# Optimization experiments

Hardware: AMD Instinct MI355X
Metric: run time of the kernel (lower is better)

Reference implementation:

```python
import jax, jax.numpy as jnp
import numpy as np

D = 64
H = 4
HD = D // H
N_MOL, E_MOL = 2048, 32768
N_PROT, E_PROT = 8192, 262144
LN_EPS = 1e-5


def _lin_params(key, d_in, d_out):
    k1, k2 = jax.random.split(key)
    lim = 1.0 / np.sqrt(d_in)
    w = jax.random.uniform(k1, (d_in, d_out), minval=-lim, maxval=lim, dtype=jnp.float32)
    b = jax.random.uniform(k2, (d_out,), minval=-lim, maxval=lim, dtype=jnp.float32)
    return w, b


def setup_inputs() -> dict:
    key = jax.random.key(0)
    ks = jax.random.split(key, 20)
    inp = {
        'x_mol': jax.random.normal(ks[0], (N_MOL, D), dtype=jnp.float32),
        'edge_index_mol': jax.random.randint(ks[1], (2, E_MOL), 0, N_MOL),
        'edge_attr_mol': jax.random.normal(ks[2], (E_MOL, D), dtype=jnp.float32),
        'x_prot': jax.random.normal(ks[3], (N_PROT, D), dtype=jnp.float32),
        'edge_index_prot': jax.random.randint(ks[4], (2, E_PROT), 0, N_PROT),
        'edge_attr_prot': jax.random.normal(ks[5], (E_PROT, D), dtype=jnp.float32),
    }
    # GINE MLPs: Linear -> ReLU -> Linear
    inp['mol_w1'], inp['mol_b1'] = _lin_params(ks[6], D, D)
    inp['mol_w2'], inp['mol_b2'] = _lin_params(ks[7], D, D)
    inp['prot_w1'], inp['prot_b1'] = _lin_params(ks[8], D, D)
    inp['prot_w2'], inp['prot_b2'] = _lin_params(ks[9], D, D)
    # cross-attn mol->prot (query=mol, key/value=prot)
    inp['mp_wq'], inp['mp_bq'] = _lin_params(ks[10], D, D)
    inp['mp_wk'], inp['mp_bk'] = _lin_params(ks[11], D, D)
    inp['mp_wv'], inp['mp_bv'] = _lin_params(ks[12], D, D)
    # cross-attn prot->mol (query=prot, key/value=mol)
    inp['pm_wq'], inp['pm_bq'] = _lin_params(ks[13], D, D)
    inp['pm_wk'], inp['pm_bk'] = _lin_params(ks[14], D, D)
    inp['pm_wv'], inp['pm_bv'] = _lin_params(ks[15], D, D)
    # layer norms
    inp['ln_mol_g'] = jnp.ones((D,), jnp.float32)
    inp['ln_mol_b'] = jnp.zeros((D,), jnp.float32)
    inp['ln_prot_g'] = jnp.ones((D,), jnp.float32)
    inp['ln_prot_b'] = jnp.zeros((D,), jnp.float32)
    return inp


def _gine_conv(x, edge_index, edge_attr, w1, b1, w2, b2, n_nodes):
    # message: relu(x_j + edge_attr); aggregate: mean at target; update: MLP((1+eps)*x + aggr), eps=0
    src, dst = edge_index[0], edge_index[1]
    msg = jax.nn.relu(x[src] + edge_attr)                       # [E, D]
    ssum = jax.ops.segment_sum(msg, dst, num_segments=n_nodes)  # [N, D]
    cnt = jax.ops.segment_sum(jnp.ones((msg.shape[0],), msg.dtype), dst, num_segments=n_nodes)
    aggr = ssum / jnp.maximum(cnt, 1.0)[:, None]
    h = x + aggr
    h = jax.nn.relu(h @ w1 + b1) @ w2 + b2
    return h


def _cross_attn(q_nodes, k_nodes, wq, bq, wk, bk, wv, bv):
    Nq, Nk = q_nodes.shape[0], k_nodes.shape[0]
    Q = (q_nodes @ wq + bq).reshape(Nq, H, HD)
    K = (k_nodes @ wk + bk).reshape(Nk, H, HD)
    V = (k_nodes @ wv + bv).reshape(Nk, H, HD)
    scores = jnp.einsum('qhd,khd->hqk', Q, K) / np.sqrt(HD).astype(np.float32)
    attn = jax.nn.softmax(scores, axis=-1)                      # [H, Nq, Nk]
    out = jnp.einsum('hqk,khd->qhd', attn, V).reshape(Nq, D)
    return out


def _layer_norm(x, g, b):
    mu = jnp.mean(x, axis=-1, keepdims=True)
    var = jnp.mean(jnp.square(x - mu), axis=-1, keepdims=True)
    return (x - mu) * jax.lax.rsqrt(var + LN_EPS) * g + b


def reference(x_mol, edge_index_mol, edge_attr_mol, x_prot, edge_index_prot, edge_attr_prot,
              mol_w1, mol_b1, mol_w2, mol_b2, prot_w1, prot_b1, prot_w2, prot_b2,
              mp_wq, mp_bq, mp_wk, mp_bk, mp_wv, mp_bv,
              pm_wq, pm_bq, pm_wk, pm_bk, pm_wv, pm_bv,
              ln_mol_g, ln_mol_b, ln_prot_g, ln_prot_b):
    h_mol = jax.nn.relu(_gine_conv(x_mol, edge_index_mol, edge_attr_mol,
                                   mol_w1, mol_b1, mol_w2, mol_b2, x_mol.shape[0]))
    h_prot = jax.nn.relu(_gine_conv(x_prot, edge_index_prot, edge_attr_prot,
                                    prot_w1, prot_b1, prot_w2, prot_b2, x_prot.shape[0]))
    h_mol_attn = _cross_attn(h_mol, h_prot, mp_wq, mp_bq, mp_wk, mp_bk, mp_wv, mp_bv)
    h_prot_attn = _cross_attn(h_prot, h_mol, pm_wq, pm_bq, pm_wk, pm_bk, pm_wv, pm_bv)
    out_mol = _layer_norm(h_mol + h_mol_attn, ln_mol_g, ln_mol_b)
    out_prot = _layer_norm(h_prot + h_prot_attn, ln_prot_g, ln_prot_b)
    return out_mol, out_prot
```

## Files before the change

kernel.cpp:

```cpp
#include <hip/hip_runtime.h>
#include <hip/hip_bf16.h>

#define NM 2048
#define EM 32768
#define NP 8192
#define EP 262144

typedef __attribute__((ext_vector_type(8))) short short8;
typedef __attribute__((ext_vector_type(4))) float f32x4;

#define LOG2E 1.44269504088896340736f

__device__ __forceinline__ unsigned short cvt_bf16(float f) {
    __hip_bfloat16 h = __float2bfloat16(f);
    return *(unsigned short*)&h;
}
__device__ __forceinline__ unsigned int pk_bf16(float a, float b) {
    unsigned int lo = cvt_bf16(a), hi = cvt_bf16(b);
    return lo | (hi << 16);
}

__global__ __launch_bounds__(256) void hist_kernel(
    const int* __restrict__ ei_m, const int* __restrict__ ei_p,
    int* __restrict__ cnt_m, int* __restrict__ cnt_p)
{
    int idx = blockIdx.x * 256 + threadIdx.x;
    if (idx < EM) atomicAdd(&cnt_m[ei_m[EM + idx]], 1);
    int j = idx - EM;
    if (j >= 0 && j < EP) atomicAdd(&cnt_p[ei_p[EP + j]], 1);
}

__global__ __launch_bounds__(256) void scan_kernel(
    const int* __restrict__ cnt_m, const int* __restrict__ cnt_p,
    int* __restrict__ start_m, int* __restrict__ start_p,
    int* __restrict__ cur_m, int* __restrict__ cur_p)
{
    const int* cnt; int* start; int* cur; int n;
    if (blockIdx.x == 0) { cnt = cnt_m; start = start_m; cur = cur_m; n = NM; }
    else                 { cnt = cnt_p; start = start_p; cur = cur_p; n = NP; }
    int per = n >> 8;
    int tid = threadIdx.x;
    int base = tid * per;
    int s = 0;
    for (int i = 0; i < per; i++) s += cnt[base + i];
    __shared__ int wsum[4];
    int lane = tid & 63, w = tid >> 6;
    int v = s;
    #pragma unroll
    for (int off = 1; off < 64; off <<= 1) {
        int u = __shfl_up(v, off, 64);
        if (lane >= off) v += u;
    }
    if (lane == 63) wsum[w] = v;
    __syncthreads();
    int wo = 0;
    for (int i = 0; i < w; i++) wo += wsum[i];
    int run = wo + v - s;
    for (int i = 0; i < per; i++) {
        start[base + i] = run; cur[base + i] = run;
        run += cnt[base + i];
    }
    if (tid == 255) start[n] = run;
}

__global__ __launch_bounds__(256) void scatter_kernel(
    const int* __restrict__ ei_m, const int* __restrict__ ei_p,
    int* __restrict__ cur_m, int* __restrict__ cur_p,
    int* __restrict__ perm_m, int* __restrict__ perm_p,
    int* __restrict__ srcs_m, int* __restrict__ srcs_p)
{
    int idx = blockIdx.x * 256 + threadIdx.x;
    if (idx < EM) {
        int d = ei_m[EM + idx];
        int pos = atomicAdd(&cur_m[d], 1);
        perm_m[pos] = idx; srcs_m[pos] = ei_m[idx];
    }
    int j = idx - EM;
    if (j >= 0 && j < EP) {
        int d = ei_p[EP + j];
        int pos = atomicAdd(&cur_p[d], 1);
        perm_p[pos] = j; srcs_p[pos] = ei_p[j];
    }
}

__global__ __launch_bounds__(256) void node_aggr_kernel(
    const float* __restrict__ x_m, const float* __restrict__ ea_m,
    const int* __restrict__ start_m, const int* __restrict__ perm_m, const int* __restrict__ srcs_m,
    const float* __restrict__ x_p, const float* __restrict__ ea_p,
    const int* __restrict__ start_p, const int* __restrict__ perm_p, const int* __restrict__ srcs_p,
    float* __restrict__ h0_m, float* __restrict__ h0_p)
{
    int wave = threadIdx.x >> 6, lane = threadIdx.x & 63;
    int nid = blockIdx.x * 4 + wave;
    const float *x, *ea; const int *start, *perm, *srcs; float* h0; int n;
    if (nid < NM) { x = x_m; ea = ea_m; start = start_m; perm = perm_m; srcs = srcs_m; h0 = h0_m; n = nid; }
    else          { x = x_p; ea = ea_p; start = start_p; perm = perm_p; srcs = srcs_p; h0 = h0_p; n = nid - NM; }
    int b = start[n], e = start[n + 1];
    int deg = e - b;
    float acc = 0.f;
    for (int c0 = 0; c0 < deg; c0 += 64) {
        int rem = deg - c0;
        int mcount = rem < 64 ? rem : 64;
        int eL = 0, sL = 0;
        if (lane < mcount) { eL = perm[b + c0 + lane]; sL = srcs[b + c0 + lane]; }
        int j = 0;
        for (; j + 3 < mcount; j += 4) {
            int e0 = __shfl(eL, j, 64),   e1 = __shfl(eL, j + 1, 64);
            int e2 = __shfl(eL, j + 2, 64), e3 = __shfl(eL, j + 3, 64);
            int s0 = __shfl(sL, j, 64),   s1 = __shfl(sL, j + 1, 64);
            int s2 = __shfl(sL, j + 2, 64), s3 = __shfl(sL, j + 3, 64);
            float a0 = ea[(size_t)e0 * 64 + lane], a1 = ea[(size_t)e1 * 64 + lane];
            float a2 = ea[(size_t)e2 * 64 + lane], a3 = ea[(size_t)e3 * 64 + lane];
            float y0 = x[(size_t)s0 * 64 + lane], y1 = x[(size_t)s1 * 64 + lane];
            float y2 = x[(size_t)s2 * 64 + lane], y3 = x[(size_t)s3 * 64 + lane];
            acc += fmaxf(y0 + a0, 0.f);
            acc += fmaxf(y1 + a1, 0.f);
            acc += fmaxf(y2 + a2, 0.f);
            acc += fmaxf(y3 + a3, 0.f);
        }
        for (; j < mcount; ++j) {
            int e0 = __shfl(eL, j, 64);
            int s0 = __shfl(sL, j, 64);
            acc += fmaxf(x[(size_t)s0 * 64 + lane] + ea[(size_t)e0 * 64 + lane], 0.f);
        }
    }
    float aggr = acc / fmaxf((float)deg, 1.f);
    h0[(size_t)n * 64 + lane] = x[(size_t)n * 64 + lane] + aggr;
}

__global__ __launch_bounds__(256) void gine_mlp_kernel(
    const float* __restrict__ h0_m, const float* __restrict__ h0_p,
    const float* __restrict__ w1m, const float* __restrict__ b1m,
    const float* __restrict__ w2m, const float* __restrict__ b2m,
    const float* __restrict__ w1p, const float* __restrict__ b1p,
    const float* __restrict__ w2p, const float* __restrict__ b2p,
    float* __restrict__ hm, float* __restrict__ hp)
{
    const float *h0, *w1, *b1, *w2, *b2; float* out; int row0;
    if (blockIdx.x < NM / 16) {
        h0 = h0_m; w1 = w1m; b1 = b1m; w2 = w2m; b2 = b2m; out = hm;
        row0 = blockIdx.x * 16;
    } else {
        h0 = h0_p; w1 = w1p; b1 = b1p; w2 = w2p; b2 = b2p; out = hp;
        row0 = (blockIdx.x - NM / 16) * 16;
    }
    __shared__ float sW1[4096], sW2[4096], sb1[64], sb2[64];
    __shared__ float sh0[16][64], sh1[16][64];
    int t = threadIdx.x;
    for (int i = t; i < 4096; i += 256) { sW1[i] = w1[i]; sW2[i] = w2[i]; }
    if (t < 64) { sb1[t] = b1[t]; sb2[t] = b2[t]; }
    for (int i = t; i < 16 * 64; i += 256) {
        int r = i >> 6, c = i & 63;
        sh0[r][c] = h0[(size_t)(row0 + r) * 64 + c];
    }
    __syncthreads();
    int j = t & 63, rs = t >> 6;
    for (int r = rs; r < 16; r += 4) {
        float a = sb1[j];
        #pragma unroll
        for (int c = 0; c < 64; c++) a += sh0[r][c] * sW1[c * 64 + j];
        sh1[r][j] = fmaxf(a, 0.0f);
    }
    __syncthreads();
    for (int r = rs; r < 16; r += 4) {
        float a = sb2[j];
        #pragma unroll
        for (int c = 0; c < 64; c++) a += sh1[r][c] * sW2[c * 64 + j];
        out[(size_t)(row0 + r) * 64 + j] = fmaxf(a, 0.0f);
    }
}

__global__ __launch_bounds__(256) void qkv_bf16_kernel(
    const float* __restrict__ hm, const float* __restrict__ hp,
    const float* __restrict__ wq_m, const float* __restrict__ bq_m,
    const float* __restrict__ wk_m, const float* __restrict__ bk_m,
    const float* __restrict__ wv_m, const float* __restrict__ bv_m,
    const float* __restrict__ wq_p, const float* __restrict__ bq_p,
    const float* __restrict__ wk_p, const float* __restrict__ bk_p,
    const float* __restrict__ wv_p, const float* __restrict__ bv_p,
    unsigned short* __restrict__ Qm, unsigned short* __restrict__ Km, unsigned short* __restrict__ Vtm,
    unsigned short* __restrict__ Qp, unsigned short* __restrict__ Kp, unsigned short* __restrict__ Vtp)
{
    const float *x, *wq, *bq, *wk, *bk, *wv, *bv;
    unsigned short *Q, *K, *Vt; int row0, N;
    if (blockIdx.x < NM / 16) {
        x = hm; wq = wq_m; bq = bq_m; wk = wk_m; bk = bk_m; wv = wv_m; bv = bv_m;
        Q = Qm; K = Km; Vt = Vtm; N = NM; row0 = blockIdx.x * 16;
    } else {
        x = hp; wq = wq_p; bq = bq_p; wk = wk_p; bk = bk_p; wv = wv_p; bv = bv_p;
        Q = Qp; K = Kp; Vt = Vtp; N = NP; row0 = (blockIdx.x - NM / 16) * 16;
    }
    __shared__ float sWq[4096], sWk[4096], sWv[4096];
    __shared__ float sbq[64], sbk[64], sbv[64];
    __shared__ float sh0[16][64];
    int t = threadIdx.x;
    for (int i = t; i < 4096; i += 256) { sWq[i] = wq[i]; sWk[i] = wk[i]; sWv[i] = wv[i]; }
    if (t < 64) { sbq[t] = bq[t]; sbk[t] = bk[t]; sbv[t] = bv[t]; }
    for (int i = t; i < 16 * 64; i += 256) {
        int r = i >> 6, c = i & 63;
        sh0[r][c] = x[(size_t)(row0 + r) * 64 + c];
    }
    __syncthreads();
    int j = t & 63, rs = t >> 6;
    for (int r = rs; r < 16; r += 4) {
        float aq = sbq[j], ak = sbk[j], av = sbv[j];
        #pragma unroll
        for (int c = 0; c < 64; c++) {
            float h = sh0[r][c];
            aq += h * sWq[c * 64 + j];
            ak += h * sWk[c * 64 + j];
            av += h * sWv[c * 64 + j];
        }
        size_t o = (size_t)(row0 + r) * 64 + j;
        Q[o] = cvt_bf16(aq * (0.25f * LOG2E));
        K[o] = cvt_bf16(ak);
        Vt[(size_t)j * N + row0 + r] = cvt_bf16(av);
    }
}

__global__ __launch_bounds__(256) void attn_partial_kernel(
    const unsigned short* __restrict__ Q, const unsigned short* __restrict__ K,
    const unsigned short* __restrict__ Vt, float* __restrict__ partial,
    int Nk, int ncbits)
{
    __shared__ unsigned int plds[4][16][20];
    int t = threadIdx.x;
    int wave = t >> 6;
    int lane = t & 63;
    int qrow = lane & 15;
    int quad = lane >> 4;
    int NC = 1 << ncbits;
    int task = blockIdx.x * 4 + wave;
    int chunk = task & (NC - 1);
    int tmp = task >> ncbits;
    int h = tmp & 3;
    int qt = tmp >> 2;

    short8 qf = {};
    if (quad < 2)
        qf = *(const short8*)(Q + ((size_t)(qt * 16 + qrow)) * 64 + h * 16 + quad * 8);

    float m = -3.0e38f, l = 0.0f;
    f32x4 acc = {0.f, 0.f, 0.f, 0.f};
    const f32x4 zero4 = {0.f, 0.f, 0.f, 0.f};
    int kbase = chunk * 1024;
    const unsigned short* vrow = Vt + ((size_t)(h * 16 + qrow)) * Nk;

    short8 kf0n = {}, kf1n = {}, vfn;
    {
        int key0 = kbase;
        if (quad < 2) {
            kf0n = *(const short8*)(K + ((size_t)(key0 + qrow)) * 64 + h * 16 + quad * 8);
            kf1n = *(const short8*)(K + ((size_t)(key0 + 16 + qrow)) * 64 + h * 16 + quad * 8);
        }
        vfn = *(const short8*)(vrow + key0 + quad * 8);
    }

    for (int it = 0; it < 32; ++it) {
        short8 kf0 = kf0n, kf1 = kf1n, vf = vfn;
        if (it < 31) {
            int key0 = kbase + (it + 1) * 32;
            if (quad < 2) {
                kf0n = *(const short8*)(K + ((size_t)(key0 + qrow)) * 64 + h * 16 + quad * 8);
                kf1n = *(const short8*)(K + ((size_t)(key0 + 16 + qrow)) * 64 + h * 16 + quad * 8);
            }
            vfn = *(const short8*)(vrow + key0 + quad * 8);
        }

        f32x4 s0 = __builtin_amdgcn_mfma_f32_16x16x32_bf16(kf0, qf, zero4, 0, 0, 0);
        f32x4 s1 = __builtin_amdgcn_mfma_f32_16x16x32_bf16(kf1, qf, zero4, 0, 0, 0);

        float tmax = fmaxf(fmaxf(fmaxf(s0.x, s0.y), fmaxf(s0.z, s0.w)),
                           fmaxf(fmaxf(s1.x, s1.y), fmaxf(s1.z, s1.w)));
        tmax = fmaxf(tmax, __shfl_xor(tmax, 16, 64));
        tmax = fmaxf(tmax, __shfl_xor(tmax, 32, 64));
        float mnew = fmaxf(m, tmax);
        float alpha = exp2f(m - mnew);
        float p00 = exp2f(s0.x - mnew), p01 = exp2f(s0.y - mnew);
        float p02 = exp2f(s0.z - mnew), p03 = exp2f(s0.w - mnew);
        float p10 = exp2f(s1.x - mnew), p11 = exp2f(s1.y - mnew);
        float p12 = exp2f(s1.z - mnew), p13 = exp2f(s1.w - mnew);
        l = l * alpha + (((p00 + p01) + (p02 + p03)) + ((p10 + p11) + (p12 + p13)));
        acc.x *= alpha; acc.y *= alpha; acc.z *= alpha; acc.w *= alpha;

        plds[wave][qrow][quad * 2]     = pk_bf16(p00, p01);
        plds[wave][qrow][quad * 2 + 1] = pk_bf16(p02, p03);
        plds[wave][qrow][8 + quad * 2]     = pk_bf16(p10, p11);
        plds[wave][qrow][8 + quad * 2 + 1] = pk_bf16(p12, p13);
        short8 pf = *(short8*)&plds[wave][qrow][quad * 4];

        acc = __builtin_amdgcn_mfma_f32_16x16x32_bf16(vf, pf, acc, 0, 0, 0);
        m = mnew;
    }

    float ltot = l + __shfl_xor(l, 16, 64);
    ltot += __shfl_xor(ltot, 32, 64);

    float* pb = partial + (size_t)task * 288;
    *(f32x4*)&pb[qrow * 16 + quad * 4] = acc;
    if (quad == 0) { pb[256 + qrow] = m; pb[272 + qrow] = ltot; }
}

__global__ __launch_bounds__(256) void merge_ln_kernel(
    const float* __restrict__ partial, const float* __restrict__ hbuf,
    const float* __restrict__ g, const float* __restrict__ bia,
    float* __restrict__ out, int NC)
{
    int row = blockIdx.x * 4 + (threadIdx.x >> 6);
    int c = threadIdx.x & 63;
    int hi = c >> 4, d = c & 15;
    int qt = row >> 4, ql = row & 15;
    const float* base = partial + (size_t)(qt * 4 + hi) * NC * 288;
    float M = -3.0e38f;
    for (int cc = 0; cc < NC; ++cc) M = fmaxf(M, base[cc * 288 + 256 + ql]);
    float L = 0.0f, A = 0.0f;
    for (int cc = 0; cc < NC; ++cc) {
        float w = exp2f(base[cc * 288 + 256 + ql] - M);
        L += base[cc * 288 + 272 + ql] * w;
        A += base[cc * 288 + ql * 16 + d] * w;
    }
    float v = hbuf[(size_t)row * 64 + c] + A / L;
    float s = v;
    #pragma unroll
    for (int o = 32; o >= 1; o >>= 1) s += __shfl_xor(s, o, 64);
    float mu = s * (1.0f / 64.0f);
    float dv = v - mu;
    float sq = dv * dv;
    #pragma unroll
    for (int o = 32; o >= 1; o >>= 1) sq += __shfl_xor(sq, o, 64);
    float var = sq * (1.0f / 64.0f);
    out[(size_t)row * 64 + c] = dv * rsqrtf(var + 1e-5f) * g[c] + bia[c];
}

extern "C" void kernel_launch(void* const* d_in, const int* in_sizes, int n_in,
                              void* d_out, int out_size, void* d_ws, size_t ws_size,
                              hipStream_t stream)
{
    const float* x_mol   = (const float*)d_in[0];
    const int*   ei_mol  = (const int*)  d_in[1];
    const float* ea_mol  = (const float*)d_in[2];
    const float* x_prot  = (const float*)d_in[3];
    const int*   ei_prot = (const int*)  d_in[4];
    const float* ea_prot = (const float*)d_in[5];
    const float* mol_w1  = (const float*)d_in[6];
    const float* mol_b1  = (const float*)d_in[7];
    const float* mol_w2  = (const float*)d_in[8];
    const float* mol_b2  = (const float*)d_in[9];
    const float* prot_w1 = (const float*)d_in[10];
    const float* prot_b1 = (const float*)d_in[11];
    const float* prot_w2 = (const float*)d_in[12];
    const float* prot_b2 = (const float*)d_in[13];
    const float* mp_wq = (const float*)d_in[14]; const float* mp_bq = (const float*)d_in[15];
    const float* mp_wk = (const float*)d_in[16]; const float* mp_bk = (const float*)d_in[17];
    const float* mp_wv = (const float*)d_in[18]; const float* mp_bv = (const float*)d_in[19];
    const float* pm_wq = (const float*)d_in[20]; const float* pm_bq = (const float*)d_in[21];
    const float* pm_wk = (const float*)d_in[22]; const float* pm_bk = (const float*)d_in[23];
    const float* pm_wv = (const float*)d_in[24]; const float* pm_bv = (const float*)d_in[25];
    const float* ln_mol_g  = (const float*)d_in[26];
    const float* ln_mol_b  = (const float*)d_in[27];
    const float* ln_prot_g = (const float*)d_in[28];
    const float* ln_prot_b = (const float*)d_in[29];

    float* ws = (float*)d_ws;
    float* h_mol   = ws;
    float* h_prot  = h_mol + 131072;
    float* partial = h_prot + 524288;
    float* h0_mol  = partial;
    float* h0_prot = h0_mol + 131072;
    int* ip      = (int*)(partial + 1179648);
    int* cnt_m   = ip;
    int* cnt_p   = cnt_m + 2048;
    int* start_m = cnt_p + 8192;
    int* start_p = start_m + 2052;
    int* cur_m   = start_p + 8196;
    int* cur_p   = cur_m + 2048;
    int* perm_m  = cur_p + 8192;
    int* perm_p  = perm_m + 32768;
    int* srcs_m  = perm_p + 262144;
    int* srcs_p  = srcs_m + 32768;
    unsigned short* bf = (unsigned short*)(srcs_p + 262144);
    unsigned short* Qm  = bf;
    unsigned short* Km  = Qm + 131072;
    unsigned short* Vtm = Km + 131072;
    unsigned short* Qp  = Vtm + 131072;
    unsigned short* Kp  = Qp + 524288;
    unsigned short* Vtp = Kp + 524288;

    hipMemsetAsync(cnt_m, 0, (size_t)(2048 + 8192) * sizeof(int), stream);

    const int EB = (EM + EP) / 256;
    hist_kernel<<<EB, 256, 0, stream>>>(ei_mol, ei_prot, cnt_m, cnt_p);
    scan_kernel<<<2, 256, 0, stream>>>(cnt_m, cnt_p, start_m, start_p, cur_m, cur_p);
    scatter_kernel<<<EB, 256, 0, stream>>>(ei_mol, ei_prot, cur_m, cur_p, perm_m, perm_p, srcs_m, srcs_p);
    node_aggr_kernel<<<(NM + NP) / 4, 256, 0, stream>>>(
        x_mol, ea_mol, start_m, perm_m, srcs_m,
        x_prot, ea_prot, start_p, perm_p, srcs_p, h0_mol, h0_prot);

    gine_mlp_kernel<<<(NM + NP) / 16, 256, 0, stream>>>(
        h0_mol, h0_prot, mol_w1, mol_b1, mol_w2, mol_b2,
        prot_w1, prot_b1, prot_w2, prot_b2, h_mol, h_prot);

    qkv_bf16_kernel<<<(NM + NP) / 16, 256, 0, stream>>>(
        h_mol, h_prot,
        mp_wq, mp_bq, pm_wk, pm_bk, pm_wv, pm_bv,
        pm_wq, pm_bq, mp_wk, mp_bk, mp_wv, mp_bv,
        Qm, Km, Vtm, Qp, Kp, Vtp);

    float* out = (float*)d_out;

    attn_partial_kernel<<<1024, 256, 0, stream>>>(Qm, Kp, Vtp, partial, NP, 3);
    merge_ln_kernel<<<NM / 4, 256, 0, stream>>>(partial, h_mol, ln_mol_g, ln_mol_b, out, 8);

    attn_partial_kernel<<<1024, 256, 0, stream>>>(Qp, Km, Vtm, partial, NM, 1);
    merge_ln_kernel<<<NP / 4, 256, 0, stream>>>(partial, h_prot, ln_prot_g, ln_prot_b, out + 131072, 2);
}
```

Before: 333.2 us.

## Fuse both attention directions and merges into single launches; pack edge indices

```diff
diff --git a/kernel.cpp b/kernel.cpp
--- a/kernel.cpp
+++ b/kernel.cpp
@@ -1,5 +1,4 @@
 #include <hip/hip_runtime.h>
-#include <hip/hip_bf16.h>
 
 #define NM 2048
 #define EM 32768
@@ -11,13 +10,16 @@
 
 #define LOG2E 1.44269504088896340736f
 
+__device__ __forceinline__ float e2(float x) { return __builtin_amdgcn_exp2f(x); }
+__device__ __forceinline__ unsigned int pk_bf16(float a, float b) {
+    unsigned int ua = __float_as_uint(a) + 0x8000u;
+    unsigned int ub = __float_as_uint(b) + 0x8000u;
+    return __builtin_amdgcn_perm(ua, ub, 0x03020706u);
+}
 __device__ __forceinline__ unsigned short cvt_bf16(float f) {
-    __hip_bfloat16 h = __float2bfloat16(f);
-    return *(unsigned short*)&h;
-}
-__device__ __forceinline__ unsigned int pk_bf16(float a, float b) {
-    unsigned int lo = cvt_bf16(a), hi = cvt_bf16(b);
-    return lo | (hi << 16);
+    unsigned int u = __float_as_uint(f);
+    u = (u + 0x7fff + ((u >> 16) & 1)) >> 16;
+    return (unsigned short)u;
 }
 
 __global__ __launch_bounds__(256) void hist_kernel(
@@ -66,62 +68,62 @@
 __global__ __launch_bounds__(256) void scatter_kernel(
     const int* __restrict__ ei_m, const int* __restrict__ ei_p,
     int* __restrict__ cur_m, int* __restrict__ cur_p,
-    int* __restrict__ perm_m, int* __restrict__ perm_p,
-    int* __restrict__ srcs_m, int* __restrict__ srcs_p)
+    int* __restrict__ pidx_m, int* __restrict__ pidx_p)
 {
     int idx = blockIdx.x * 256 + threadIdx.x;
     if (idx < EM) {
         int d = ei_m[EM + idx];
         int pos = atomicAdd(&cur_m[d], 1);
-        perm_m[pos] = idx; srcs_m[pos] = ei_m[idx];
+        pidx_m[pos] = (idx << 11) | ei_m[idx];
     }
     int j = idx - EM;
     if (j >= 0 && j < EP) {
         int d = ei_p[EP + j];
         int pos = atomicAdd(&cur_p[d], 1);
-        perm_p[pos] = j; srcs_p[pos] = ei_p[j];
+        pidx_p[pos] = (j << 13) | ei_p[j];
     }
 }
 
 __global__ __launch_bounds__(256) void node_aggr_kernel(
     const float* __restrict__ x_m, const float* __restrict__ ea_m,
-    const int* __restrict__ start_m, const int* __restrict__ perm_m, const int* __restrict__ srcs_m,
+    const int* __restrict__ start_m, const int* __restrict__ pidx_m,
     const float* __restrict__ x_p, const float* __restrict__ ea_p,
-    const int* __restrict__ start_p, const int* __restrict__ perm_p, const int* __restrict__ srcs_p,
+    const int* __restrict__ start_p, const int* __restrict__ pidx_p,
     float* __restrict__ h0_m, float* __restrict__ h0_p)
 {
     int wave = threadIdx.x >> 6, lane = threadIdx.x & 63;
     int nid = blockIdx.x * 4 + wave;
-    const float *x, *ea; const int *start, *perm, *srcs; float* h0; int n;
-    if (nid < NM) { x = x_m; ea = ea_m; start = start_m; perm = perm_m; srcs = srcs_m; h0 = h0_m; n = nid; }
-    else          { x = x_p; ea = ea_p; start = start_p; perm = perm_p; srcs = srcs_p; h0 = h0_p; n = nid - NM; }
+    const float *x, *ea; const int *start, *pidx; float* h0; int n, sh, msk;
+    if (nid < NM) { x = x_m; ea = ea_m; start = start_m; pidx = pidx_m; h0 = h0_m; n = nid; sh = 11; msk = 2047; }
+    else          { x = x_p; ea = ea_p; start = start_p; pidx = pidx_p; h0 = h0_p; n = nid - NM; sh = 13; msk = 8191; }
     int b = start[n], e = start[n + 1];
     int deg = e - b;
     float acc = 0.f;
     for (int c0 = 0; c0 < deg; c0 += 64) {
         int rem = deg - c0;
         int mcount = rem < 64 ? rem : 64;
-        int eL = 0, sL = 0;
-        if (lane < mcount) { eL = perm[b + c0 + lane]; sL = srcs[b + c0 + lane]; }
+        int pk = 0;
+        if (lane < mcount) pk = pidx[b + c0 + lane];
         int j = 0;
         for (; j + 3 < mcount; j += 4) {
-            int e0 = __shfl(eL, j, 64),   e1 = __shfl(eL, j + 1, 64);
-            int e2 = __shfl(eL, j + 2, 64), e3 = __shfl(eL, j + 3, 64);
-            int s0 = __shfl(sL, j, 64),   s1 = __shfl(sL, j + 1, 64);
-            int s2 = __shfl(sL, j + 2, 64), s3 = __shfl(sL, j + 3, 64);
-            float a0 = ea[(size_t)e0 * 64 + lane], a1 = ea[(size_t)e1 * 64 + lane];
-            float a2 = ea[(size_t)e2 * 64 + lane], a3 = ea[(size_t)e3 * 64 + lane];
-            float y0 = x[(size_t)s0 * 64 + lane], y1 = x[(size_t)s1 * 64 + lane];
-            float y2 = x[(size_t)s2 * 64 + lane], y3 = x[(size_t)s3 * 64 + lane];
+            int v0 = __shfl(pk, j, 64),     v1 = __shfl(pk, j + 1, 64);
+            int v2 = __shfl(pk, j + 2, 64), v3 = __shfl(pk, j + 3, 64);
+            float a0 = ea[(size_t)(((unsigned)v0) >> sh) * 64 + lane];
+            float a1 = ea[(size_t)(((unsigned)v1) >> sh) * 64 + lane];
+            float a2 = ea[(size_t)(((unsigned)v2) >> sh) * 64 + lane];
+            float a3 = ea[(size_t)(((unsigned)v3) >> sh) * 64 + lane];
+            float y0 = x[(size_t)(v0 & msk) * 64 + lane];
+            float y1 = x[(size_t)(v1 & msk) * 64 + lane];
+            float y2 = x[(size_t)(v2 & msk) * 64 + lane];
+            float y3 = x[(size_t)(v3 & msk) * 64 + lane];
             acc += fmaxf(y0 + a0, 0.f);
             acc += fmaxf(y1 + a1, 0.f);
             acc += fmaxf(y2 + a2, 0.f);
             acc += fmaxf(y3 + a3, 0.f);
         }
         for (; j < mcount; ++j) {
-            int e0 = __shfl(eL, j, 64);
-            int s0 = __shfl(sL, j, 64);
-            acc += fmaxf(x[(size_t)s0 * 64 + lane] + ea[(size_t)e0 * 64 + lane], 0.f);
+            int v0 = __shfl(pk, j, 64);
+            acc += fmaxf(x[(size_t)(v0 & msk) * 64 + lane] + ea[(size_t)(((unsigned)v0) >> sh) * 64 + lane], 0.f);
         }
     }
     float aggr = acc / fmaxf((float)deg, 1.f);
@@ -218,10 +220,12 @@
     }
 }
 
-__global__ __launch_bounds__(256) void attn_partial_kernel(
-    const unsigned short* __restrict__ Q, const unsigned short* __restrict__ K,
-    const unsigned short* __restrict__ Vt, float* __restrict__ partial,
-    int Nk, int ncbits)
+__global__ __launch_bounds__(256) void attn_kernel(
+    const unsigned short* __restrict__ Qm, const unsigned short* __restrict__ Km,
+    const unsigned short* __restrict__ Vtm,
+    const unsigned short* __restrict__ Qp, const unsigned short* __restrict__ Kp,
+    const unsigned short* __restrict__ Vtp,
+    float* __restrict__ partial)
 {
     __shared__ unsigned int plds[4][16][20];
     int t = threadIdx.x;
@@ -229,10 +233,13 @@
     int lane = t & 63;
     int qrow = lane & 15;
     int quad = lane >> 4;
-    int NC = 1 << ncbits;
-    int task = blockIdx.x * 4 + wave;
-    int chunk = task & (NC - 1);
-    int tmp = task >> ncbits;
+    int T = blockIdx.x * 4 + wave;
+
+    const unsigned short *Q, *K, *Vt; int Nk, ncb, tloc;
+    if (T < 4096) { Q = Qm; K = Kp; Vt = Vtp; Nk = NP; ncb = 3; tloc = T; }
+    else          { Q = Qp; K = Km; Vt = Vtm; Nk = NM; ncb = 1; tloc = T - 4096; }
+    int chunk = tloc & ((1 << ncb) - 1);
+    int tmp = tloc >> ncb;
     int h = tmp & 3;
     int qt = tmp >> 2;
 
@@ -248,12 +255,11 @@
 
     short8 kf0n = {}, kf1n = {}, vfn;
     {
-        int key0 = kbase;
         if (quad < 2) {
-            kf0n = *(const short8*)(K + ((size_t)(key0 + qrow)) * 64 + h * 16 + quad * 8);
-            kf1n = *(const short8*)(K + ((size_t)(key0 + 16 + qrow)) * 64 + h * 16 + quad * 8);
+            kf0n = *(const short8*)(K + ((size_t)(kbase + qrow)) * 64 + h * 16 + quad * 8);
+            kf1n = *(const short8*)(K + ((size_t)(kbase + 16 + qrow)) * 64 + h * 16 + quad * 8);
         }
-        vfn = *(const short8*)(vrow + key0 + quad * 8);
+        vfn = *(const short8*)(vrow + kbase + quad * 8);
     }
 
     for (int it = 0; it < 32; ++it) {
@@ -275,18 +281,18 @@
         tmax = fmaxf(tmax, __shfl_xor(tmax, 16, 64));
         tmax = fmaxf(tmax, __shfl_xor(tmax, 32, 64));
         float mnew = fmaxf(m, tmax);
-        float alpha = exp2f(m - mnew);
-        float p00 = exp2f(s0.x - mnew), p01 = exp2f(s0.y - mnew);
-        float p02 = exp2f(s0.z - mnew), p03 = exp2f(s0.w - mnew);
-        float p10 = exp2f(s1.x - mnew), p11 = exp2f(s1.y - mnew);
-        float p12 = exp2f(s1.z - mnew), p13 = exp2f(s1.w - mnew);
+        float alpha = e2(m - mnew);
+        float p00 = e2(s0.x - mnew), p01 = e2(s0.y - mnew);
+        float p02 = e2(s0.z - mnew), p03 = e2(s0.w - mnew);
+        float p10 = e2(s1.x - mnew), p11 = e2(s1.y - mnew);
+        float p12 = e2(s1.z - mnew), p13 = e2(s1.w - mnew);
         l = l * alpha + (((p00 + p01) + (p02 + p03)) + ((p10 + p11) + (p12 + p13)));
         acc.x *= alpha; acc.y *= alpha; acc.z *= alpha; acc.w *= alpha;
 
-        plds[wave][qrow][quad * 2]     = pk_bf16(p00, p01);
-        plds[wave][qrow][quad * 2 + 1] = pk_bf16(p02, p03);
-        plds[wave][qrow][8 + quad * 2]     = pk_bf16(p10, p11);
-        plds[wave][qrow][8 + quad * 2 + 1] = pk_bf16(p12, p13);
+        uint2 w0; w0.x = pk_bf16(p00, p01); w0.y = pk_bf16(p02, p03);
+        uint2 w1; w1.x = pk_bf16(p10, p11); w1.y = pk_bf16(p12, p13);
+        *(uint2*)&plds[wave][qrow][quad * 2] = w0;
+        *(uint2*)&plds[wave][qrow][8 + quad * 2] = w1;
         short8 pf = *(short8*)&plds[wave][qrow][quad * 4];
 
         acc = __builtin_amdgcn_mfma_f32_16x16x32_bf16(vf, pf, acc, 0, 0, 0);
@@ -296,40 +302,46 @@
     float ltot = l + __shfl_xor(l, 16, 64);
     ltot += __shfl_xor(ltot, 32, 64);
 
-    float* pb = partial + (size_t)task * 288;
+    float* pb = partial + (size_t)T * 288;
     *(f32x4*)&pb[qrow * 16 + quad * 4] = acc;
     if (quad == 0) { pb[256 + qrow] = m; pb[272 + qrow] = ltot; }
 }
 
 __global__ __launch_bounds__(256) void merge_ln_kernel(
-    const float* __restrict__ partial, const float* __restrict__ hbuf,
-    const float* __restrict__ g, const float* __restrict__ bia,
-    float* __restrict__ out, int NC)
-{
-    int row = blockIdx.x * 4 + (threadIdx.x >> 6);
-    int c = threadIdx.x & 63;
+    const float* __restrict__ partial,
+    const float* __restrict__ h_m, const float* __restrict__ h_p,
+    const float* __restrict__ gm, const float* __restrict__ bm,
+    const float* __restrict__ gp, const float* __restrict__ bp_,
+    float* __restrict__ out)
+{
+    int t = threadIdx.x;
+    int grow = blockIdx.x * 4 + (t >> 6);
+    int c = t & 63;
+    const float *pbase, *hbuf, *g, *bb; float* o; int NC, row;
+    if (grow < NM) { pbase = partial;               hbuf = h_m; g = gm; bb = bm;  o = out;             NC = 8; row = grow; }
+    else           { pbase = partial + 4096 * 288;  hbuf = h_p; g = gp; bb = bp_; o = out + NM * 64;   NC = 2; row = grow - NM; }
     int hi = c >> 4, d = c & 15;
     int qt = row >> 4, ql = row & 15;
-    const float* base = partial + (size_t)(qt * 4 + hi) * NC * 288;
+    const float* base = pbase + (size_t)(qt * 4 + hi) * NC * 288;
     float M = -3.0e38f;
     for (int cc = 0; cc < NC; ++cc) M = fmaxf(M, base[cc * 288 + 256 + ql]);
     float L = 0.0f, A = 0.0f;
     for (int cc = 0; cc < NC; ++cc) {
-        float w = exp2f(base[cc * 288 + 256 + ql] - M);
+        float w = e2(base[cc * 288 + 256 + ql] - M);
         L += base[cc * 288 + 272 + ql] * w;
         A += base[cc * 288 + ql * 16 + d] * w;
     }
     float v = hbuf[(size_t)row * 64 + c] + A / L;
     float s = v;
     #pragma unroll
-    for (int o = 32; o >= 1; o >>= 1) s += __shfl_xor(s, o, 64);
+    for (int o2 = 32; o2 >= 1; o2 >>= 1) s += __shfl_xor(s, o2, 64);
     float mu = s * (1.0f / 64.0f);
     float dv = v - mu;
     float sq = dv * dv;
     #pragma unroll
-    for (int o = 32; o >= 1; o >>= 1) sq += __shfl_xor(sq, o, 64);
+    for (int o2 = 32; o2 >= 1; o2 >>= 1) sq += __shfl_xor(sq, o2, 64);
     float var = sq * (1.0f / 64.0f);
-    out[(size_t)row * 64 + c] = dv * rsqrtf(var + 1e-5f) * g[c] + bia[c];
+    o[(size_t)row * 64 + c] = dv * rsqrtf(var + 1e-5f) * g[c] + bb[c];
 }
 
 extern "C" void kernel_launch(void* const* d_in, const int* in_sizes, int n_in,
@@ -367,18 +379,16 @@
     float* partial = h_prot + 524288;
     float* h0_mol  = partial;
     float* h0_prot = h0_mol + 131072;
-    int* ip      = (int*)(partial + 1179648);
+    int* ip      = (int*)(partial + 2359296);
     int* cnt_m   = ip;
     int* cnt_p   = cnt_m + 2048;
     int* start_m = cnt_p + 8192;
     int* start_p = start_m + 2052;
     int* cur_m   = start_p + 8196;
     int* cur_p   = cur_m + 2048;
-    int* perm_m  = cur_p + 8192;
-    int* perm_p  = perm_m + 32768;
-    int* srcs_m  = perm_p + 262144;
-    int* srcs_p  = srcs_m + 32768;
-    unsigned short* bf = (unsigned short*)(srcs_p + 262144);
+    int* pidx_m  = cur_p + 8192;
+    int* pidx_p  = pidx_m + 32768;
+    unsigned short* bf = (unsigned short*)(pidx_p + 262144);
     unsigned short* Qm  = bf;
     unsigned short* Km  = Qm + 131072;
     unsigned short* Vtm = Km + 131072;
@@ -391,10 +401,10 @@
     const int EB = (EM + EP) / 256;
     hist_kernel<<<EB, 256, 0, stream>>>(ei_mol, ei_prot, cnt_m, cnt_p);
     scan_kernel<<<2, 256, 0, stream>>>(cnt_m, cnt_p, start_m, start_p, cur_m, cur_p);
-    scatter_kernel<<<EB, 256, 0, stream>>>(ei_mol, ei_prot, cur_m, cur_p, perm_m, perm_p, srcs_m, srcs_p);
+    scatter_kernel<<<EB, 256, 0, stream>>>(ei_mol, ei_prot, cur_m, cur_p, pidx_m, pidx_p);
     node_aggr_kernel<<<(NM + NP) / 4, 256, 0, stream>>>(
-        x_mol, ea_mol, start_m, perm_m, srcs_m,
-        x_prot, ea_prot, start_p, perm_p, srcs_p, h0_mol, h0_prot);
+        x_mol, ea_mol, start_m, pidx_m,
+        x_prot, ea_prot, start_p, pidx_p, h0_mol, h0_prot);
 
     gine_mlp_kernel<<<(NM + NP) / 16, 256, 0, stream>>>(
         h0_mol, h0_prot, mol_w1, mol_b1, mol_w2, mol_b2,
@@ -406,11 +416,9 @@
         pm_wq, pm_bq, mp_wk, mp_bk, mp_wv, mp_bv,
         Qm, Km, Vtm, Qp, Kp, Vtp);
 
+    attn_kernel<<<2048, 256, 0, stream>>>(Qm, Km, Vtm, Qp, Kp, Vtp, partial);
+
     float* out = (float*)d_out;
-
-    attn_partial_kernel<<<1024, 256, 0, stream>>>(Qm, Kp, Vtp, partial, NP, 3);
-    merge_ln_kernel<<<NM / 4, 256, 0, stream>>>(partial, h_mol, ln_mol_g, ln_mol_b, out, 8);
-
-    attn_partial_kernel<<<1024, 256, 0, stream>>>(Qp, Km, Vtm, partial, NM, 1);
-    merge_ln_kernel<<<NP / 4, 256, 0, stream>>>(partial, h_prot, ln_prot_g, ln_prot_b, out + 131072, 2);
-}
+    merge_ln_kernel<<<(NM + NP) / 4, 256, 0, stream>>>(
+        partial, h_mol, h_prot, ln_mol_g, ln_mol_b, ln_prot_g, ln_prot_b, out);
+}
```

After: 323.3 us. 3.0% less time.
